# Kernel tuning notes

Hardware: AMD Instinct MI355X
Metric: run time of the kernel (lower is better)

Reference implementation:

```python
import jax, jax.numpy as jnp
import numpy as np

N = 50000          # nodes
E = 800000         # directed edges (before self-loops)
F_IN = 256
HIDS = 32
HEADS = 8
N_CLASSES = 40
NEG_SLOPE = 0.2    # PyG GATConv default leaky_relu slope


def setup_inputs() -> dict:
    key = jax.random.key(0)
    ks = jax.random.split(key, 10)
    x = jax.random.normal(ks[0], (N, F_IN), dtype=jnp.float32)
    edge_index = jax.random.randint(ks[1], (2, E), 0, N, dtype=jnp.int32)
    # conv1: F_IN -> HIDS per head, HEADS heads, concat=True
    W1 = jax.random.normal(ks[2], (F_IN, HEADS * HIDS), dtype=jnp.float32) * (1.0 / np.sqrt(F_IN))
    a1_src = jax.random.normal(ks[3], (HEADS, HIDS), dtype=jnp.float32) * 0.1
    a1_dst = jax.random.normal(ks[4], (HEADS, HIDS), dtype=jnp.float32) * 0.1
    b1 = jnp.zeros((HEADS * HIDS,), dtype=jnp.float32)
    # conv2: HEADS*HIDS -> N_CLASSES, 1 head, concat=False
    W2 = jax.random.normal(ks[5], (HEADS * HIDS, N_CLASSES), dtype=jnp.float32) * (1.0 / np.sqrt(HEADS * HIDS))
    a2_src = jax.random.normal(ks[6], (1, N_CLASSES), dtype=jnp.float32) * 0.1
    a2_dst = jax.random.normal(ks[7], (1, N_CLASSES), dtype=jnp.float32) * 0.1
    b2 = jnp.zeros((N_CLASSES,), dtype=jnp.float32)
    return {"x": x, "edge_index": edge_index, "W1": W1, "a1_src": a1_src,
            "a1_dst": a1_dst, "b1": b1, "W2": W2, "a2_src": a2_src,
            "a2_dst": a2_dst, "b2": b2}


def _gat_conv(x, src, dst, W, a_src, a_dst, bias, heads, concat):
    n = x.shape[0]
    c = W.shape[1] // heads
    xw = (x @ W).reshape(n, heads, c)                       # [N,H,C]
    alpha_s = jnp.einsum('nhc,hc->nh', xw, a_src)           # [N,H]
    alpha_d = jnp.einsum('nhc,hc->nh', xw, a_dst)
    e = alpha_s[src] + alpha_d[dst]                         # [Etot,H]
    e = jnp.where(e >= 0, e, NEG_SLOPE * e)                 # leaky_relu
    # segment softmax over incoming edges of each destination node
    m = jax.ops.segment_max(e, dst, num_segments=n)         # [N,H]
    ex = jnp.exp(e - m[dst])
    denom = jax.ops.segment_sum(ex, dst, num_segments=n)    # [N,H]
    alpha = ex / denom[dst]                                 # [Etot,H]
    out = jax.ops.segment_sum(alpha[:, :, None] * xw[src], dst, num_segments=n)  # [N,H,C]
    if concat:
        out = out.reshape(n, heads * c)
    else:
        out = out.mean(axis=1)
    return out + bias


def reference(x, edge_index, W1, a1_src, a1_dst, b1, W2, a2_src, a2_dst, b2):
    n = x.shape[0]
    # add self-loops (PyG GATConv default)
    loop = jnp.arange(n, dtype=edge_index.dtype)
    src = jnp.concatenate([edge_index[0], loop])
    dst = jnp.concatenate([edge_index[1], loop])
    # dropout(p=0.6) layers are identity in eval mode
    h = _gat_conv(x, src, dst, W1, a1_src, a1_dst, b1, HEADS, True)
    h = jax.nn.elu(h)
    out = _gat_conv(h, src, dst, W2, a2_src, a2_dst, b2, 1, False)
    return out
```

## Files before the change

kernel.cpp:

```cpp
#include <hip/hip_runtime.h>
#include <hip/hip_bf16.h>

#define NNODES 50000
#define NPAD   50048
#define NEDGES 800000
#define ETOT   (NEDGES + NNODES)
#define FIN    256
#define HIDS   32
#define HEADS  8
#define NCLS   40
#define NEG    0.2f

#define SCAN_B 256
#define NSCB   ((NNODES + SCAN_B - 1) / SCAN_B)
#define NTILE1 ((NNODES + 63) / 64)

typedef __attribute__((ext_vector_type(8))) short bf16x8;
typedef __attribute__((ext_vector_type(4))) float f32x4;

__device__ __forceinline__ ushort f2bf(float f) {
  unsigned u = __float_as_uint(f);
  unsigned r = (u + 0x7fffu + ((u >> 16) & 1u)) >> 16;
  return (ushort)r;
}
__device__ __forceinline__ float bf2f(ushort u) {
  return __uint_as_float(((unsigned)u) << 16);
}
__device__ __forceinline__ float bflo(unsigned u) { return __uint_as_float(u << 16); }
__device__ __forceinline__ float bfhi(unsigned u) { return __uint_as_float(u & 0xffff0000u); }

__global__ __launch_bounds__(256) void prep_k(
    const float* __restrict__ W1, const float* __restrict__ W2,
    const float* __restrict__ a1src, const float* __restrict__ a1dst,
    const float* __restrict__ a2src, const float* __restrict__ a2dst,
    ushort* __restrict__ w1t, ushort* __restrict__ w2t,
    int* __restrict__ cnt, ushort* __restrict__ hb) {
  int b = blockIdx.x, t = threadIdx.x;
  if (b < 256) {
    int k = b, n = t;
    w1t[(size_t)n * 256 + k] = f2bf(W1[(size_t)k * 256 + n]);
  } else if (b < 272) {
    int j = b - 256, k = t;
    const float* av = (j < 8) ? (a1src + j * 32) : (a1dst + (j - 8) * 32);
    int nb = (j < 8) ? j * 32 : (j - 8) * 32;
    float s = 0.f;
#pragma unroll
    for (int c = 0; c < 32; ++c) s += W1[(size_t)k * 256 + nb + c] * av[c];
    w1t[(size_t)(256 + j) * 256 + k] = f2bf(s);
  } else if (b < 320) {
    w1t[(size_t)b * 256 + t] = 0;
  } else if (b < 384) {
    int n = b - 320, k = t;
    ushort v;
    if (n < NCLS) {
      v = f2bf(W2[(size_t)k * NCLS + n]);
    } else if (n == 40) {
      float s = 0.f;
#pragma unroll
      for (int c = 0; c < NCLS; ++c) s += W2[(size_t)k * NCLS + c] * a2src[c];
      v = f2bf(s);
    } else if (n == 41) {
      float s = 0.f;
#pragma unroll
      for (int c = 0; c < NCLS; ++c) s += W2[(size_t)k * NCLS + c] * a2dst[c];
      v = f2bf(s);
    } else {
      v = 0;
    }
    w2t[(size_t)n * 256 + k] = v;
  } else if (b < 580) {
    int i = (b - 384) * 256 + t;
    if (i < NNODES) cnt[i] = 0;
  } else {
    int r = NNODES + (b - 580);
    hb[(size_t)r * 256 + t] = 0;
  }
}

__global__ __launch_bounds__(256) void gemm1_mfma(
    const float* __restrict__ x, const ushort* __restrict__ w1t,
    ushort* __restrict__ xw1s, float* __restrict__ a1s, float* __restrict__ a1d) {
  __shared__ ushort As[64 * 40];
  __shared__ ushort Bs[320 * 40];
  const int tid = threadIdx.x;
  const int m0 = blockIdx.x * 64;
  const int w = tid >> 6, l = tid & 63, lr = l & 15, lq = l >> 4;
  f32x4 acc[4][5];
#pragma unroll
  for (int i = 0; i < 4; ++i)
#pragma unroll
    for (int j = 0; j < 5; ++j) acc[i][j] = (f32x4)0.f;

  for (int k0 = 0; k0 < 256; k0 += 32) {
    {
      int row = tid >> 2, kg = (tid & 3) * 8;
      int gr = m0 + row;
      bf16x8 av;
      if (gr < NNODES) {
        const float4* xp = (const float4*)(x + (size_t)gr * 256 + k0 + kg);
        float4 p0 = xp[0], p1 = xp[1];
        av[0] = (short)f2bf(p0.x); av[1] = (short)f2bf(p0.y);
        av[2] = (short)f2bf(p0.z); av[3] = (short)f2bf(p0.w);
        av[4] = (short)f2bf(p1.x); av[5] = (short)f2bf(p1.y);
        av[6] = (short)f2bf(p1.z); av[7] = (short)f2bf(p1.w);
      } else {
        av = (bf16x8)0;
      }
      *(bf16x8*)&As[row * 40 + kg] = av;
    }
#pragma unroll
    for (int p = 0; p < 5; ++p) {
      int idx = tid + p * 256;
      int n = idx >> 2, kg = (idx & 3) * 8;
      *(bf16x8*)&Bs[n * 40 + kg] = *(const bf16x8*)(w1t + (size_t)n * 256 + k0 + kg);
    }
    __syncthreads();
    bf16x8 af[4], bfr[5];
#pragma unroll
    for (int mt = 0; mt < 4; ++mt)
      af[mt] = *(const bf16x8*)&As[(mt * 16 + lr) * 40 + lq * 8];
#pragma unroll
    for (int nt = 0; nt < 5; ++nt) {
      int tile = nt * 4 + w;
      bfr[nt] = *(const bf16x8*)&Bs[(tile * 16 + lr) * 40 + lq * 8];
    }
#pragma unroll
    for (int mt = 0; mt < 4; ++mt)
#pragma unroll
      for (int nt = 0; nt < 5; ++nt)
        acc[mt][nt] = __builtin_amdgcn_mfma_f32_16x16x32_bf16(af[mt], bfr[nt], acc[mt][nt], 0, 0, 0);
    __syncthreads();
  }
#pragma unroll
  for (int mt = 0; mt < 4; ++mt)
#pragma unroll
    for (int nt = 0; nt < 5; ++nt) {
      int tile = nt * 4 + w;
      if (tile < 16) {
        int colc = tile * 16 + lr;
        int s = colc >> 5, c = colc & 31;
#pragma unroll
        for (int r = 0; r < 4; ++r) {
          int row = m0 + mt * 16 + lq * 4 + r;
          xw1s[((size_t)s * NPAD + row) * 32 + c] = f2bf(acc[mt][nt][r]);
        }
      } else if (tile == 16) {
#pragma unroll
        for (int r = 0; r < 4; ++r) {
          int row = m0 + mt * 16 + lq * 4 + r;
          if (lr < 8) a1s[(size_t)row * 8 + lr] = acc[mt][nt][r];
          else        a1d[(size_t)row * 8 + (lr - 8)] = acc[mt][nt][r];
        }
      }
    }
}

__global__ __launch_bounds__(256) void gemm2_mfma(
    const ushort* __restrict__ hb, const ushort* __restrict__ w2t,
    ushort* __restrict__ xw2b, float* __restrict__ a2s, float* __restrict__ a2d) {
  const int tid = threadIdx.x;
  const int w = tid >> 6, l = tid & 63, lr = l & 15, lq = l >> 4;
  const int row0 = blockIdx.x * 64 + w * 16;
  f32x4 acc[3];
#pragma unroll
  for (int i = 0; i < 3; ++i) acc[i] = (f32x4)0.f;
#pragma unroll
  for (int ks = 0; ks < 8; ++ks) {
    int k0 = ks * 32;
    bf16x8 af = *(const bf16x8*)(hb + (size_t)(row0 + lr) * 256 + k0 + lq * 8);
#pragma unroll
    for (int nt = 0; nt < 3; ++nt) {
      bf16x8 bfr = *(const bf16x8*)(w2t + (size_t)(nt * 16 + lr) * 256 + k0 + lq * 8);
      acc[nt] = __builtin_amdgcn_mfma_f32_16x16x32_bf16(af, bfr, acc[nt], 0, 0, 0);
    }
  }
#pragma unroll
  for (int nt = 0; nt < 3; ++nt) {
    int colc = nt * 16 + lr;
#pragma unroll
    for (int r = 0; r < 4; ++r) {
      int row = row0 + lq * 4 + r;
      if (colc < NCLS)      xw2b[(size_t)row * 40 + colc] = f2bf(acc[nt][r]);
      else if (colc == 40)  a2s[row] = acc[nt][r];
      else if (colc == 41)  a2d[row] = acc[nt][r];
    }
  }
}

__global__ __launch_bounds__(256) void hist_k(const int* __restrict__ dstA, int* __restrict__ cnt) {
  int e = blockIdx.x * 256 + threadIdx.x;
  if (e >= ETOT) return;
  int d = (e < NEDGES) ? dstA[e] : (e - NEDGES);
  atomicAdd(&cnt[d], 1);
}

__global__ __launch_bounds__(SCAN_B) void scan1_k(const int* __restrict__ deg,
                                                  int* __restrict__ row_ptr,
                                                  int* __restrict__ bsum) {
  __shared__ int sm[SCAN_B];
  int b = blockIdx.x, t = threadIdx.x;
  int idx = b * SCAN_B + t;
  int v = (idx < NNODES) ? deg[idx] : 0;
  sm[t] = v;
  __syncthreads();
#pragma unroll
  for (int off = 1; off < SCAN_B; off <<= 1) {
    int u = (t >= off) ? sm[t - off] : 0;
    __syncthreads();
    sm[t] += u;
    __syncthreads();
  }
  if (idx < NNODES) row_ptr[idx + 1] = sm[t];
  if (t == SCAN_B - 1) bsum[b] = sm[t];
}

__global__ __launch_bounds__(256) void scan2_k(int* __restrict__ bsum) {
  __shared__ int sm[256];
  int t = threadIdx.x;
  sm[t] = (t < NSCB) ? bsum[t] : 0;
  __syncthreads();
#pragma unroll
  for (int off = 1; off < 256; off <<= 1) {
    int u = (t >= off) ? sm[t - off] : 0;
    __syncthreads();
    sm[t] += u;
    __syncthreads();
  }
  if (t < NSCB) bsum[t] = (t > 0) ? sm[t - 1] : 0;
}

__global__ __launch_bounds__(SCAN_B) void scan3_k(const int* __restrict__ bsum,
                                                  int* __restrict__ row_ptr) {
  int b = blockIdx.x, t = threadIdx.x;
  int idx = b * SCAN_B + t;
  if (idx < NNODES) row_ptr[idx + 1] += bsum[b];
  if (b == 0 && t == 0) row_ptr[0] = 0;
}

__global__ __launch_bounds__(256) void scatter_k(const int* __restrict__ srcA, const int* __restrict__ dstA,
                                                 const int* __restrict__ row_ptr, int* __restrict__ cnt,
                                                 int* __restrict__ col, int* __restrict__ edst) {
  int e = blockIdx.x * 256 + threadIdx.x;
  if (e >= ETOT) return;
  int s, d;
  if (e < NEDGES) { s = srcA[e]; d = dstA[e]; }
  else { s = d = e - NEDGES; }
  int old = atomicSub(&cnt[d], 1);
  int pos = row_ptr[d] + old - 1;
  col[pos] = s;
  edst[pos] = d;
}

__global__ __launch_bounds__(256) void ew_k(
    const float* __restrict__ a1s, const float* __restrict__ a1d,
    const int* __restrict__ col, const int* __restrict__ edst,
    float* __restrict__ ew) {
  int pos = blockIdx.x * 256 + threadIdx.x;
  if (pos >= ETOT) return;
  int src = col[pos], dst = edst[pos];
  const float4* sp = (const float4*)(a1s + (size_t)src * 8);
  const float4* dp = (const float4*)(a1d + (size_t)dst * 8);
  float4 s0 = sp[0], s1 = sp[1];
  float4 d0 = dp[0], d1 = dp[1];
  float e[8] = {s0.x + d0.x, s0.y + d0.y, s0.z + d0.z, s0.w + d0.w,
                s1.x + d1.x, s1.y + d1.y, s1.z + d1.z, s1.w + d1.w};
#pragma unroll
  for (int h = 0; h < 8; ++h) {
    float v = e[h];
    v = fmaxf(v, 0.f) + NEG * fminf(v, 0.f);
    ew[(size_t)h * ETOT + pos] = __expf(v);
  }
}

__global__ __launch_bounds__(256) void ew2_k(
    const float* __restrict__ a2s, const float* __restrict__ a2d,
    const int* __restrict__ col, const int* __restrict__ edst,
    float* __restrict__ ew2) {
  int pos = blockIdx.x * 256 + threadIdx.x;
  if (pos >= ETOT) return;
  float e = a2s[col[pos]] + a2d[edst[pos]];
  e = fmaxf(e, 0.f) + NEG * fminf(e, 0.f);
  ew2[pos] = __expf(e);
}

__global__ __launch_bounds__(256) void agg1_k(
    const ushort* __restrict__ xw1s, const float* __restrict__ ew,
    const int* __restrict__ row_ptr, const int* __restrict__ col,
    const float* __restrict__ b1, ushort* __restrict__ hb) {
  const int b = blockIdx.x;
  const int s = b & 7;
  const int t = threadIdx.x;
  const int node = (b >> 3) * 64 + (t >> 2);
  const int q = t & 3;
  if (node >= NNODES) return;
  const ushort* xs = xw1s + (size_t)s * NPAD * 32 + q * 8;
  const float* ws = ew + (size_t)s * ETOT;
  int i = row_ptr[node];
  const int end = row_ptr[node + 1];
  float den = 0.f;
  float c0 = 0.f, c1 = 0.f, c2 = 0.f, c3 = 0.f, c4 = 0.f, c5 = 0.f, c6 = 0.f, c7 = 0.f;
  for (; i + 4 <= end; i += 4) {
    int s0 = col[i], s1 = col[i + 1], s2 = col[i + 2], s3 = col[i + 3];
    float w0 = ws[i], w1 = ws[i + 1], w2 = ws[i + 2], w3 = ws[i + 3];
    uint4 u0 = *(const uint4*)(xs + (size_t)s0 * 32);
    uint4 u1 = *(const uint4*)(xs + (size_t)s1 * 32);
    uint4 u2 = *(const uint4*)(xs + (size_t)s2 * 32);
    uint4 u3 = *(const uint4*)(xs + (size_t)s3 * 32);
    den += (w0 + w1) + (w2 + w3);
    c0 += w0 * bflo(u0.x) + w1 * bflo(u1.x) + w2 * bflo(u2.x) + w3 * bflo(u3.x);
    c1 += w0 * bfhi(u0.x) + w1 * bfhi(u1.x) + w2 * bfhi(u2.x) + w3 * bfhi(u3.x);
    c2 += w0 * bflo(u0.y) + w1 * bflo(u1.y) + w2 * bflo(u2.y) + w3 * bflo(u3.y);
    c3 += w0 * bfhi(u0.y) + w1 * bfhi(u1.y) + w2 * bfhi(u2.y) + w3 * bfhi(u3.y);
    c4 += w0 * bflo(u0.z) + w1 * bflo(u1.z) + w2 * bflo(u2.z) + w3 * bflo(u3.z);
    c5 += w0 * bfhi(u0.z) + w1 * bfhi(u1.z) + w2 * bfhi(u2.z) + w3 * bfhi(u3.z);
    c6 += w0 * bflo(u0.w) + w1 * bflo(u1.w) + w2 * bflo(u2.w) + w3 * bflo(u3.w);
    c7 += w0 * bfhi(u0.w) + w1 * bfhi(u1.w) + w2 * bfhi(u2.w) + w3 * bfhi(u3.w);
  }
  for (; i < end; ++i) {
    int s0 = col[i];
    float w0 = ws[i];
    uint4 u0 = *(const uint4*)(xs + (size_t)s0 * 32);
    den += w0;
    c0 += w0 * bflo(u0.x); c1 += w0 * bfhi(u0.x);
    c2 += w0 * bflo(u0.y); c3 += w0 * bfhi(u0.y);
    c4 += w0 * bflo(u0.z); c5 += w0 * bfhi(u0.z);
    c6 += w0 * bflo(u0.w); c7 += w0 * bfhi(u0.w);
  }
  const float inv = 1.f / den;
  const float4 bv0 = *reinterpret_cast<const float4*>(b1 + s * 32 + q * 8);
  const float4 bv1 = *reinterpret_cast<const float4*>(b1 + s * 32 + q * 8 + 4);
  float o[8];
  o[0] = c0 * inv + bv0.x; o[1] = c1 * inv + bv0.y;
  o[2] = c2 * inv + bv0.z; o[3] = c3 * inv + bv0.w;
  o[4] = c4 * inv + bv1.x; o[5] = c5 * inv + bv1.y;
  o[6] = c6 * inv + bv1.z; o[7] = c7 * inv + bv1.w;
  uint4 pk;
  unsigned r[4];
#pragma unroll
  for (int p = 0; p < 4; ++p) {
    float a = o[2 * p],     va = (a > 0.f) ? a : expm1f(a);
    float c = o[2 * p + 1], vc = (c > 0.f) ? c : expm1f(c);
    r[p] = (unsigned)f2bf(va) | ((unsigned)f2bf(vc) << 16);
  }
  pk.x = r[0]; pk.y = r[1]; pk.z = r[2]; pk.w = r[3];
  *(uint4*)(hb + (size_t)node * 256 + s * 32 + q * 8) = pk;
}

__global__ __launch_bounds__(320) void agg2_k(
    const ushort* __restrict__ xw2b, const float* __restrict__ ew2,
    const int* __restrict__ row_ptr, const int* __restrict__ col,
    const float* __restrict__ b2, float* __restrict__ out) {
  const int t = threadIdx.x;
  const int lane = t & 63;
  const int g = t >> 6;
  const int node = blockIdx.x * 64 + lane;
  if (node >= NNODES) return;
  const int c0off = g * 8;
  int i = row_ptr[node];
  const int end = row_ptr[node + 1];
  float den = 0.f;
  float c0 = 0.f, c1 = 0.f, c2 = 0.f, c3 = 0.f, c4 = 0.f, c5 = 0.f, c6 = 0.f, c7 = 0.f;
  for (; i + 4 <= end; i += 4) {
    int s0 = col[i], s1 = col[i + 1], s2 = col[i + 2], s3 = col[i + 3];
    float w0 = ew2[i], w1 = ew2[i + 1], w2 = ew2[i + 2], w3 = ew2[i + 3];
    uint4 u0 = *(const uint4*)(xw2b + (size_t)s0 * 40 + c0off);
    uint4 u1 = *(const uint4*)(xw2b + (size_t)s1 * 40 + c0off);
    uint4 u2 = *(const uint4*)(xw2b + (size_t)s2 * 40 + c0off);
    uint4 u3 = *(const uint4*)(xw2b + (size_t)s3 * 40 + c0off);
    den += (w0 + w1) + (w2 + w3);
    c0 += w0 * bflo(u0.x) + w1 * bflo(u1.x) + w2 * bflo(u2.x) + w3 * bflo(u3.x);
    c1 += w0 * bfhi(u0.x) + w1 * bfhi(u1.x) + w2 * bfhi(u2.x) + w3 * bfhi(u3.x);
    c2 += w0 * bflo(u0.y) + w1 * bflo(u1.y) + w2 * bflo(u2.y) + w3 * bflo(u3.y);
    c3 += w0 * bfhi(u0.y) + w1 * bfhi(u1.y) + w2 * bfhi(u2.y) + w3 * bfhi(u3.y);
    c4 += w0 * bflo(u0.z) + w1 * bflo(u1.z) + w2 * bflo(u2.z) + w3 * bflo(u3.z);
    c5 += w0 * bfhi(u0.z) + w1 * bfhi(u1.z) + w2 * bfhi(u2.z) + w3 * bfhi(u3.z);
    c6 += w0 * bflo(u0.w) + w1 * bflo(u1.w) + w2 * bflo(u2.w) + w3 * bflo(u3.w);
    c7 += w0 * bfhi(u0.w) + w1 * bfhi(u1.w) + w2 * bfhi(u2.w) + w3 * bfhi(u3.w);
  }
  for (; i < end; ++i) {
    int s0 = col[i];
    float w0 = ew2[i];
    uint4 u0 = *(const uint4*)(xw2b + (size_t)s0 * 40 + c0off);
    den += w0;
    c0 += w0 * bflo(u0.x); c1 += w0 * bfhi(u0.x);
    c2 += w0 * bflo(u0.y); c3 += w0 * bfhi(u0.y);
    c4 += w0 * bflo(u0.z); c5 += w0 * bfhi(u0.z);
    c6 += w0 * bflo(u0.w); c7 += w0 * bfhi(u0.w);
  }
  const float inv = 1.f / den;
  const float* bp = b2 + c0off;
  float o[8];
  o[0] = c0 * inv + bp[0]; o[1] = c1 * inv + bp[1];
  o[2] = c2 * inv + bp[2]; o[3] = c3 * inv + bp[3];
  o[4] = c4 * inv + bp[4]; o[5] = c5 * inv + bp[5];
  o[6] = c6 * inv + bp[6]; o[7] = c7 * inv + bp[7];
  float* op = out + (size_t)node * 40 + c0off;
  *(float4*)op = make_float4(o[0], o[1], o[2], o[3]);
  *(float4*)(op + 4) = make_float4(o[4], o[5], o[6], o[7]);
}

extern "C" void kernel_launch(void* const* d_in, const int* in_sizes, int n_in,
                              void* d_out, int out_size, void* d_ws, size_t ws_size,
                              hipStream_t stream) {
  const float* x     = (const float*)d_in[0];
  const int*   ei    = (const int*)d_in[1];
  const float* W1    = (const float*)d_in[2];
  const float* a1src = (const float*)d_in[3];
  const float* a1dst = (const float*)d_in[4];
  const float* b1    = (const float*)d_in[5];
  const float* W2    = (const float*)d_in[6];
  const float* a2src = (const float*)d_in[7];
  const float* a2dst = (const float*)d_in[8];
  const float* b2    = (const float*)d_in[9];
  float* out = (float*)d_out;

  const int* srcA = ei;
  const int* dstA = ei + NEDGES;

  ushort* w1t  = (ushort*)d_ws;
  ushort* w2t  = w1t + (size_t)320 * 256;
  ushort* xw1s = w2t + (size_t)64 * 256;
  ushort* hb   = xw1s + (size_t)NPAD * 256;
  ushort* xw2b = hb + (size_t)NPAD * 256;
  float* a1s   = (float*)(xw2b + (size_t)NPAD * 40);
  float* a1d   = a1s + (size_t)NPAD * 8;
  float* a2s   = a1d + (size_t)NPAD * 8;
  float* a2d   = a2s + NPAD;
  float* ew    = a2d + NPAD;
  float* ew2   = ew + (size_t)8 * ETOT;
  int* row_ptr = (int*)(ew2 + ETOT);
  int* cnt     = row_ptr + (NNODES + 1);
  int* col     = cnt + NNODES;
  int* edst    = col + ETOT;
  int* bsum    = edst + ETOT;

  prep_k<<<628, 256, 0, stream>>>(W1, W2, a1src, a1dst, a2src, a2dst, w1t, w2t, cnt, hb);

  gemm1_mfma<<<NPAD / 64, 256, 0, stream>>>(x, w1t, xw1s, a1s, a1d);

  hist_k<<<(ETOT + 255) / 256, 256, 0, stream>>>(dstA, cnt);
  scan1_k<<<NSCB, SCAN_B, 0, stream>>>(cnt, row_ptr, bsum);
  scan2_k<<<1, 256, 0, stream>>>(bsum);
  scan3_k<<<NSCB, SCAN_B, 0, stream>>>(bsum, row_ptr);
  scatter_k<<<(ETOT + 255) / 256, 256, 0, stream>>>(srcA, dstA, row_ptr, cnt, col, edst);

  ew_k<<<(ETOT + 255) / 256, 256, 0, stream>>>(a1s, a1d, col, edst, ew);

  agg1_k<<<NTILE1 * 8, 256, 0, stream>>>(xw1s, ew, row_ptr, col, b1, hb);

  gemm2_mfma<<<NPAD / 64, 256, 0, stream>>>(hb, w2t, xw2b, a2s, a2d);

  ew2_k<<<(ETOT + 255) / 256, 256, 0, stream>>>(a2s, a2d, col, edst, ew2);

  agg2_k<<<NTILE1, 320, 0, stream>>>(xw2b, ew2, row_ptr, col, b2, out);
}
```

Baseline: 264.5 us.

## Fuse edge-weight computation into scatter and agg2, drop edst array

Computes layer-1 edge weights inside the CSR scatter kernel using the original src/dst, so the separate ew_k pass and the edst array are removed. Layer-2 edge weights are now computed on the fly inside agg2 from a2s/a2d, which eliminates ew2_k and the ew2 buffer at the cost of some redundant exp work across the five channel groups. It also marks col and ew loads in the aggregation kernels as nontemporal. The scatter's ew stores are now random rather than coalesced.

```diff
diff --git a/kernel.cpp b/kernel.cpp
--- a/kernel.cpp
+++ b/kernel.cpp
@@ -237,9 +237,11 @@
   if (b == 0 && t == 0) row_ptr[0] = 0;
 }
 
-__global__ __launch_bounds__(256) void scatter_k(const int* __restrict__ srcA, const int* __restrict__ dstA,
-                                                 const int* __restrict__ row_ptr, int* __restrict__ cnt,
-                                                 int* __restrict__ col, int* __restrict__ edst) {
+__global__ __launch_bounds__(256) void scatter_ew_k(
+    const int* __restrict__ srcA, const int* __restrict__ dstA,
+    const int* __restrict__ row_ptr, int* __restrict__ cnt,
+    const float* __restrict__ a1s, const float* __restrict__ a1d,
+    int* __restrict__ col, float* __restrict__ ew) {
   int e = blockIdx.x * 256 + threadIdx.x;
   if (e >= ETOT) return;
   int s, d;
@@ -248,39 +250,18 @@
   int old = atomicSub(&cnt[d], 1);
   int pos = row_ptr[d] + old - 1;
   col[pos] = s;
-  edst[pos] = d;
-}
-
-__global__ __launch_bounds__(256) void ew_k(
-    const float* __restrict__ a1s, const float* __restrict__ a1d,
-    const int* __restrict__ col, const int* __restrict__ edst,
-    float* __restrict__ ew) {
-  int pos = blockIdx.x * 256 + threadIdx.x;
-  if (pos >= ETOT) return;
-  int src = col[pos], dst = edst[pos];
-  const float4* sp = (const float4*)(a1s + (size_t)src * 8);
-  const float4* dp = (const float4*)(a1d + (size_t)dst * 8);
+  const float4* sp = (const float4*)(a1s + (size_t)s * 8);
+  const float4* dp = (const float4*)(a1d + (size_t)d * 8);
   float4 s0 = sp[0], s1 = sp[1];
   float4 d0 = dp[0], d1 = dp[1];
-  float e[8] = {s0.x + d0.x, s0.y + d0.y, s0.z + d0.z, s0.w + d0.w,
-                s1.x + d1.x, s1.y + d1.y, s1.z + d1.z, s1.w + d1.w};
+  float ev[8] = {s0.x + d0.x, s0.y + d0.y, s0.z + d0.z, s0.w + d0.w,
+                 s1.x + d1.x, s1.y + d1.y, s1.z + d1.z, s1.w + d1.w};
 #pragma unroll
   for (int h = 0; h < 8; ++h) {
-    float v = e[h];
+    float v = ev[h];
     v = fmaxf(v, 0.f) + NEG * fminf(v, 0.f);
     ew[(size_t)h * ETOT + pos] = __expf(v);
   }
-}
-
-__global__ __launch_bounds__(256) void ew2_k(
-    const float* __restrict__ a2s, const float* __restrict__ a2d,
-    const int* __restrict__ col, const int* __restrict__ edst,
-    float* __restrict__ ew2) {
-  int pos = blockIdx.x * 256 + threadIdx.x;
-  if (pos >= ETOT) return;
-  float e = a2s[col[pos]] + a2d[edst[pos]];
-  e = fmaxf(e, 0.f) + NEG * fminf(e, 0.f);
-  ew2[pos] = __expf(e);
 }
 
 __global__ __launch_bounds__(256) void agg1_k(
@@ -300,8 +281,14 @@
   float den = 0.f;
   float c0 = 0.f, c1 = 0.f, c2 = 0.f, c3 = 0.f, c4 = 0.f, c5 = 0.f, c6 = 0.f, c7 = 0.f;
   for (; i + 4 <= end; i += 4) {
-    int s0 = col[i], s1 = col[i + 1], s2 = col[i + 2], s3 = col[i + 3];
-    float w0 = ws[i], w1 = ws[i + 1], w2 = ws[i + 2], w3 = ws[i + 3];
+    int s0 = __builtin_nontemporal_load(col + i);
+    int s1 = __builtin_nontemporal_load(col + i + 1);
+    int s2 = __builtin_nontemporal_load(col + i + 2);
+    int s3 = __builtin_nontemporal_load(col + i + 3);
+    float w0 = __builtin_nontemporal_load(ws + i);
+    float w1 = __builtin_nontemporal_load(ws + i + 1);
+    float w2 = __builtin_nontemporal_load(ws + i + 2);
+    float w3 = __builtin_nontemporal_load(ws + i + 3);
     uint4 u0 = *(const uint4*)(xs + (size_t)s0 * 32);
     uint4 u1 = *(const uint4*)(xs + (size_t)s1 * 32);
     uint4 u2 = *(const uint4*)(xs + (size_t)s2 * 32);
@@ -317,8 +304,8 @@
     c7 += w0 * bfhi(u0.w) + w1 * bfhi(u1.w) + w2 * bfhi(u2.w) + w3 * bfhi(u3.w);
   }
   for (; i < end; ++i) {
-    int s0 = col[i];
-    float w0 = ws[i];
+    int s0 = __builtin_nontemporal_load(col + i);
+    float w0 = __builtin_nontemporal_load(ws + i);
     uint4 u0 = *(const uint4*)(xs + (size_t)s0 * 32);
     den += w0;
     c0 += w0 * bflo(u0.x); c1 += w0 * bfhi(u0.x);
@@ -347,7 +334,7 @@
 }
 
 __global__ __launch_bounds__(320) void agg2_k(
-    const ushort* __restrict__ xw2b, const float* __restrict__ ew2,
+    const ushort* __restrict__ xw2b, const float* __restrict__ a2s, const float* __restrict__ a2d,
     const int* __restrict__ row_ptr, const int* __restrict__ col,
     const float* __restrict__ b2, float* __restrict__ out) {
   const int t = threadIdx.x;
@@ -356,13 +343,24 @@
   const int node = blockIdx.x * 64 + lane;
   if (node >= NNODES) return;
   const int c0off = g * 8;
+  const float ad = a2d[node];
   int i = row_ptr[node];
   const int end = row_ptr[node + 1];
   float den = 0.f;
   float c0 = 0.f, c1 = 0.f, c2 = 0.f, c3 = 0.f, c4 = 0.f, c5 = 0.f, c6 = 0.f, c7 = 0.f;
   for (; i + 4 <= end; i += 4) {
-    int s0 = col[i], s1 = col[i + 1], s2 = col[i + 2], s3 = col[i + 3];
-    float w0 = ew2[i], w1 = ew2[i + 1], w2 = ew2[i + 2], w3 = ew2[i + 3];
+    int s0 = __builtin_nontemporal_load(col + i);
+    int s1 = __builtin_nontemporal_load(col + i + 1);
+    int s2 = __builtin_nontemporal_load(col + i + 2);
+    int s3 = __builtin_nontemporal_load(col + i + 3);
+    float e0 = a2s[s0] + ad;
+    float e1 = a2s[s1] + ad;
+    float e2 = a2s[s2] + ad;
+    float e3 = a2s[s3] + ad;
+    float w0 = __expf(fmaxf(e0, 0.f) + NEG * fminf(e0, 0.f));
+    float w1 = __expf(fmaxf(e1, 0.f) + NEG * fminf(e1, 0.f));
+    float w2 = __expf(fmaxf(e2, 0.f) + NEG * fminf(e2, 0.f));
+    float w3 = __expf(fmaxf(e3, 0.f) + NEG * fminf(e3, 0.f));
     uint4 u0 = *(const uint4*)(xw2b + (size_t)s0 * 40 + c0off);
     uint4 u1 = *(const uint4*)(xw2b + (size_t)s1 * 40 + c0off);
     uint4 u2 = *(const uint4*)(xw2b + (size_t)s2 * 40 + c0off);
@@ -378,8 +376,9 @@
     c7 += w0 * bfhi(u0.w) + w1 * bfhi(u1.w) + w2 * bfhi(u2.w) + w3 * bfhi(u3.w);
   }
   for (; i < end; ++i) {
-    int s0 = col[i];
-    float w0 = ew2[i];
+    int s0 = __builtin_nontemporal_load(col + i);
+    float e0 = a2s[s0] + ad;
+    float w0 = __expf(fmaxf(e0, 0.f) + NEG * fminf(e0, 0.f));
     uint4 u0 = *(const uint4*)(xw2b + (size_t)s0 * 40 + c0off);
     den += w0;
     c0 += w0 * bflo(u0.x); c1 += w0 * bfhi(u0.x);
@@ -427,12 +426,10 @@
   float* a2s   = a1d + (size_t)NPAD * 8;
   float* a2d   = a2s + NPAD;
   float* ew    = a2d + NPAD;
-  float* ew2   = ew + (size_t)8 * ETOT;
-  int* row_ptr = (int*)(ew2 + ETOT);
+  int* row_ptr = (int*)(ew + (size_t)8 * ETOT);
   int* cnt     = row_ptr + (NNODES + 1);
   int* col     = cnt + NNODES;
-  int* edst    = col + ETOT;
-  int* bsum    = edst + ETOT;
+  int* bsum    = col + ETOT;
 
   prep_k<<<628, 256, 0, stream>>>(W1, W2, a1src, a1dst, a2src, a2dst, w1t, w2t, cnt, hb);
 
@@ -442,15 +439,12 @@
   scan1_k<<<NSCB, SCAN_B, 0, stream>>>(cnt, row_ptr, bsum);
   scan2_k<<<1, 256, 0, stream>>>(bsum);
   scan3_k<<<NSCB, SCAN_B, 0, stream>>>(bsum, row_ptr);
-  scatter_k<<<(ETOT + 255) / 256, 256, 0, stream>>>(srcA, dstA, row_ptr, cnt, col, edst);
-
-  ew_k<<<(ETOT + 255) / 256, 256, 0, stream>>>(a1s, a1d, col, edst, ew);
+
+  scatter_ew_k<<<(ETOT + 255) / 256, 256, 0, stream>>>(srcA, dstA, row_ptr, cnt, a1s, a1d, col, ew);
 
   agg1_k<<<NTILE1 * 8, 256, 0, stream>>>(xw1s, ew, row_ptr, col, b1, hb);
 
   gemm2_mfma<<<NPAD / 64, 256, 0, stream>>>(hb, w2t, xw2b, a2s, a2d);
 
-  ew2_k<<<(ETOT + 255) / 256, 256, 0, stream>>>(a2s, a2d, col, edst, ew2);
-
-  agg2_k<<<NTILE1, 320, 0, stream>>>(xw2b, ew2, row_ptr, col, b2, out);
-}
+  agg2_k<<<NTILE1, 320, 0, stream>>>(xw2b, a2s, a2d, row_ptr, col, b2, out);
+}
```

After: 389.3 us. 1.47x slower.

## Fuse layer-2 edge weights into aggregation, merge scan kernels, unroll agg1 by eight

Applied to the files above, without the earlier changes.

Drops the separate ew2_k pass and computes each layer-2 edge's leaky-relu exp weight inside agg2_k from a2s[src] and a2d[node]. This removes a kernel launch and the write and read of the ETOT-sized ew2 array. It also merges scan2 and scan3 so every block rescans the small block-sum array itself, saving a launch at the cost of redundant work. agg1 and agg2 gain an 8-wide unrolled gather loop that issues more loads before use, at the cost of more registers. The trade is that each of the five column-group waves in agg2 now computes the exp again for every edge.

```diff
diff --git a/kernel.cpp b/kernel.cpp
--- a/kernel.cpp
+++ b/kernel.cpp
@@ -214,26 +214,22 @@
   if (t == SCAN_B - 1) bsum[b] = sm[t];
 }
 
-__global__ __launch_bounds__(256) void scan2_k(int* __restrict__ bsum) {
-  __shared__ int sm[256];
-  int t = threadIdx.x;
+__global__ __launch_bounds__(SCAN_B) void scan23_k(const int* __restrict__ bsum,
+                                                   int* __restrict__ row_ptr) {
+  __shared__ int sm[SCAN_B];
+  int b = blockIdx.x, t = threadIdx.x;
   sm[t] = (t < NSCB) ? bsum[t] : 0;
   __syncthreads();
 #pragma unroll
-  for (int off = 1; off < 256; off <<= 1) {
+  for (int off = 1; off < SCAN_B; off <<= 1) {
     int u = (t >= off) ? sm[t - off] : 0;
     __syncthreads();
     sm[t] += u;
     __syncthreads();
   }
-  if (t < NSCB) bsum[t] = (t > 0) ? sm[t - 1] : 0;
-}
-
-__global__ __launch_bounds__(SCAN_B) void scan3_k(const int* __restrict__ bsum,
-                                                  int* __restrict__ row_ptr) {
-  int b = blockIdx.x, t = threadIdx.x;
+  int offb = (b > 0) ? sm[b - 1] : 0;
   int idx = b * SCAN_B + t;
-  if (idx < NNODES) row_ptr[idx + 1] += bsum[b];
+  if (idx < NNODES) row_ptr[idx + 1] += offb;
   if (b == 0 && t == 0) row_ptr[0] = 0;
 }
 
@@ -270,17 +266,6 @@
     v = fmaxf(v, 0.f) + NEG * fminf(v, 0.f);
     ew[(size_t)h * ETOT + pos] = __expf(v);
   }
-}
-
-__global__ __launch_bounds__(256) void ew2_k(
-    const float* __restrict__ a2s, const float* __restrict__ a2d,
-    const int* __restrict__ col, const int* __restrict__ edst,
-    float* __restrict__ ew2) {
-  int pos = blockIdx.x * 256 + threadIdx.x;
-  if (pos >= ETOT) return;
-  float e = a2s[col[pos]] + a2d[edst[pos]];
-  e = fmaxf(e, 0.f) + NEG * fminf(e, 0.f);
-  ew2[pos] = __expf(e);
 }
 
 __global__ __launch_bounds__(256) void agg1_k(
@@ -299,22 +284,39 @@
   const int end = row_ptr[node + 1];
   float den = 0.f;
   float c0 = 0.f, c1 = 0.f, c2 = 0.f, c3 = 0.f, c4 = 0.f, c5 = 0.f, c6 = 0.f, c7 = 0.f;
+  for (; i + 8 <= end; i += 8) {
+    int sv[8]; float wv[8]; uint4 uv[8];
+#pragma unroll
+    for (int j = 0; j < 8; ++j) sv[j] = col[i + j];
+#pragma unroll
+    for (int j = 0; j < 8; ++j) wv[j] = ws[i + j];
+#pragma unroll
+    for (int j = 0; j < 8; ++j) uv[j] = *(const uint4*)(xs + (size_t)sv[j] * 32);
+#pragma unroll
+    for (int j = 0; j < 8; ++j) {
+      den += wv[j];
+      c0 += wv[j] * bflo(uv[j].x); c1 += wv[j] * bfhi(uv[j].x);
+      c2 += wv[j] * bflo(uv[j].y); c3 += wv[j] * bfhi(uv[j].y);
+      c4 += wv[j] * bflo(uv[j].z); c5 += wv[j] * bfhi(uv[j].z);
+      c6 += wv[j] * bflo(uv[j].w); c7 += wv[j] * bfhi(uv[j].w);
+    }
+  }
   for (; i + 4 <= end; i += 4) {
-    int s0 = col[i], s1 = col[i + 1], s2 = col[i + 2], s3 = col[i + 3];
-    float w0 = ws[i], w1 = ws[i + 1], w2 = ws[i + 2], w3 = ws[i + 3];
-    uint4 u0 = *(const uint4*)(xs + (size_t)s0 * 32);
-    uint4 u1 = *(const uint4*)(xs + (size_t)s1 * 32);
-    uint4 u2 = *(const uint4*)(xs + (size_t)s2 * 32);
-    uint4 u3 = *(const uint4*)(xs + (size_t)s3 * 32);
-    den += (w0 + w1) + (w2 + w3);
-    c0 += w0 * bflo(u0.x) + w1 * bflo(u1.x) + w2 * bflo(u2.x) + w3 * bflo(u3.x);
-    c1 += w0 * bfhi(u0.x) + w1 * bfhi(u1.x) + w2 * bfhi(u2.x) + w3 * bfhi(u3.x);
-    c2 += w0 * bflo(u0.y) + w1 * bflo(u1.y) + w2 * bflo(u2.y) + w3 * bflo(u3.y);
-    c3 += w0 * bfhi(u0.y) + w1 * bfhi(u1.y) + w2 * bfhi(u2.y) + w3 * bfhi(u3.y);
-    c4 += w0 * bflo(u0.z) + w1 * bflo(u1.z) + w2 * bflo(u2.z) + w3 * bflo(u3.z);
-    c5 += w0 * bfhi(u0.z) + w1 * bfhi(u1.z) + w2 * bfhi(u2.z) + w3 * bfhi(u3.z);
-    c6 += w0 * bflo(u0.w) + w1 * bflo(u1.w) + w2 * bflo(u2.w) + w3 * bflo(u3.w);
-    c7 += w0 * bfhi(u0.w) + w1 * bfhi(u1.w) + w2 * bfhi(u2.w) + w3 * bfhi(u3.w);
+    int sv[4]; float wv[4]; uint4 uv[4];
+#pragma unroll
+    for (int j = 0; j < 4; ++j) sv[j] = col[i + j];
+#pragma unroll
+    for (int j = 0; j < 4; ++j) wv[j] = ws[i + j];
+#pragma unroll
+    for (int j = 0; j < 4; ++j) uv[j] = *(const uint4*)(xs + (size_t)sv[j] * 32);
+#pragma unroll
+    for (int j = 0; j < 4; ++j) {
+      den += wv[j];
+      c0 += wv[j] * bflo(uv[j].x); c1 += wv[j] * bfhi(uv[j].x);
+      c2 += wv[j] * bflo(uv[j].y); c3 += wv[j] * bfhi(uv[j].y);
+      c4 += wv[j] * bflo(uv[j].z); c5 += wv[j] * bfhi(uv[j].z);
+      c6 += wv[j] * bflo(uv[j].w); c7 += wv[j] * bfhi(uv[j].w);
+    }
   }
   for (; i < end; ++i) {
     int s0 = col[i];
@@ -347,7 +349,7 @@
 }
 
 __global__ __launch_bounds__(320) void agg2_k(
-    const ushort* __restrict__ xw2b, const float* __restrict__ ew2,
+    const ushort* __restrict__ xw2b, const float* __restrict__ a2s, const float* __restrict__ a2d,
     const int* __restrict__ row_ptr, const int* __restrict__ col,
     const float* __restrict__ b2, float* __restrict__ out) {
   const int t = threadIdx.x;
@@ -356,30 +358,51 @@
   const int node = blockIdx.x * 64 + lane;
   if (node >= NNODES) return;
   const int c0off = g * 8;
+  const float ad = a2d[node];
   int i = row_ptr[node];
   const int end = row_ptr[node + 1];
   float den = 0.f;
   float c0 = 0.f, c1 = 0.f, c2 = 0.f, c3 = 0.f, c4 = 0.f, c5 = 0.f, c6 = 0.f, c7 = 0.f;
+  for (; i + 8 <= end; i += 8) {
+    int sv[8]; float ev[8]; uint4 uv[8];
+#pragma unroll
+    for (int j = 0; j < 8; ++j) sv[j] = col[i + j];
+#pragma unroll
+    for (int j = 0; j < 8; ++j) ev[j] = a2s[sv[j]] + ad;
+#pragma unroll
+    for (int j = 0; j < 8; ++j) uv[j] = *(const uint4*)(xw2b + (size_t)sv[j] * 40 + c0off);
+#pragma unroll
+    for (int j = 0; j < 8; ++j) {
+      float w = __expf(fmaxf(ev[j], 0.f) + NEG * fminf(ev[j], 0.f));
+      den += w;
+      c0 += w * bflo(uv[j].x); c1 += w * bfhi(uv[j].x);
+      c2 += w * bflo(uv[j].y); c3 += w * bfhi(uv[j].y);
+      c4 += w * bflo(uv[j].z); c5 += w * bfhi(uv[j].z);
+      c6 += w * bflo(uv[j].w); c7 += w * bfhi(uv[j].w);
+    }
+  }
   for (; i + 4 <= end; i += 4) {
-    int s0 = col[i], s1 = col[i + 1], s2 = col[i + 2], s3 = col[i + 3];
-    float w0 = ew2[i], w1 = ew2[i + 1], w2 = ew2[i + 2], w3 = ew2[i + 3];
-    uint4 u0 = *(const uint4*)(xw2b + (size_t)s0 * 40 + c0off);
-    uint4 u1 = *(const uint4*)(xw2b + (size_t)s1 * 40 + c0off);
-    uint4 u2 = *(const uint4*)(xw2b + (size_t)s2 * 40 + c0off);
-    uint4 u3 = *(const uint4*)(xw2b + (size_t)s3 * 40 + c0off);
-    den += (w0 + w1) + (w2 + w3);
-    c0 += w0 * bflo(u0.x) + w1 * bflo(u1.x) + w2 * bflo(u2.x) + w3 * bflo(u3.x);
-    c1 += w0 * bfhi(u0.x) + w1 * bfhi(u1.x) + w2 * bfhi(u2.x) + w3 * bfhi(u3.x);
-    c2 += w0 * bflo(u0.y) + w1 * bflo(u1.y) + w2 * bflo(u2.y) + w3 * bflo(u3.y);
-    c3 += w0 * bfhi(u0.y) + w1 * bfhi(u1.y) + w2 * bfhi(u2.y) + w3 * bfhi(u3.y);
-    c4 += w0 * bflo(u0.z) + w1 * bflo(u1.z) + w2 * bflo(u2.z) + w3 * bflo(u3.z);
-    c5 += w0 * bfhi(u0.z) + w1 * bfhi(u1.z) + w2 * bfhi(u2.z) + w3 * bfhi(u3.z);
-    c6 += w0 * bflo(u0.w) + w1 * bflo(u1.w) + w2 * bflo(u2.w) + w3 * bflo(u3.w);
-    c7 += w0 * bfhi(u0.w) + w1 * bfhi(u1.w) + w2 * bfhi(u2.w) + w3 * bfhi(u3.w);
+    int sv[4]; float ev[4]; uint4 uv[4];
+#pragma unroll
+    for (int j = 0; j < 4; ++j) sv[j] = col[i + j];
+#pragma unroll
+    for (int j = 0; j < 4; ++j) ev[j] = a2s[sv[j]] + ad;
+#pragma unroll
+    for (int j = 0; j < 4; ++j) uv[j] = *(const uint4*)(xw2b + (size_t)sv[j] * 40 + c0off);
+#pragma unroll
+    for (int j = 0; j < 4; ++j) {
+      float w = __expf(fmaxf(ev[j], 0.f) + NEG * fminf(ev[j], 0.f));
+      den += w;
+      c0 += w * bflo(uv[j].x); c1 += w * bfhi(uv[j].x);
+      c2 += w * bflo(uv[j].y); c3 += w * bfhi(uv[j].y);
+      c4 += w * bflo(uv[j].z); c5 += w * bfhi(uv[j].z);
+      c6 += w * bflo(uv[j].w); c7 += w * bfhi(uv[j].w);
+    }
   }
   for (; i < end; ++i) {
     int s0 = col[i];
-    float w0 = ew2[i];
+    float e0 = a2s[s0] + ad;
+    float w0 = __expf(fmaxf(e0, 0.f) + NEG * fminf(e0, 0.f));
     uint4 u0 = *(const uint4*)(xw2b + (size_t)s0 * 40 + c0off);
     den += w0;
     c0 += w0 * bflo(u0.x); c1 += w0 * bfhi(u0.x);
@@ -427,8 +450,7 @@
   float* a2s   = a1d + (size_t)NPAD * 8;
   float* a2d   = a2s + NPAD;
   float* ew    = a2d + NPAD;
-  float* ew2   = ew + (size_t)8 * ETOT;
-  int* row_ptr = (int*)(ew2 + ETOT);
+  int* row_ptr = (int*)(ew + (size_t)8 * ETOT);
   int* cnt     = row_ptr + (NNODES + 1);
   int* col     = cnt + NNODES;
   int* edst    = col + ETOT;
@@ -440,8 +462,7 @@
 
   hist_k<<<(ETOT + 255) / 256, 256, 0, stream>>>(dstA, cnt);
   scan1_k<<<NSCB, SCAN_B, 0, stream>>>(cnt, row_ptr, bsum);
-  scan2_k<<<1, 256, 0, stream>>>(bsum);
-  scan3_k<<<NSCB, SCAN_B, 0, stream>>>(bsum, row_ptr);
+  scan23_k<<<NSCB, SCAN_B, 0, stream>>>(bsum, row_ptr);
   scatter_k<<<(ETOT + 255) / 256, 256, 0, stream>>>(srcA, dstA, row_ptr, cnt, col, edst);
 
   ew_k<<<(ETOT + 255) / 256, 256, 0, stream>>>(a1s, a1d, col, edst, ew);
@@ -450,7 +471,5 @@
 
   gemm2_mfma<<<NPAD / 64, 256, 0, stream>>>(hb, w2t, xw2b, a2s, a2d);
 
-  ew2_k<<<(ETOT + 255) / 256, 256, 0, stream>>>(a2s, a2d, col, edst, ew2);
-
-  agg2_k<<<NTILE1, 320, 0, stream>>>(xw2b, ew2, row_ptr, col, b2, out);
-}
+  agg2_k<<<NTILE1, 320, 0, stream>>>(xw2b, a2s, a2d, row_ptr, col, b2, out);
+}
```

Result: no change. 267.2 us (+1.0%).
